# Performance work log

Hardware: AMD Instinct MI355X
Metric: run time of the kernel (lower is better)

The kernel has to match this reference:

```python
import jax, jax.numpy as jnp
import numpy as np
from jax import lax

INF = 1e12  # stands in for +inf background in the squared EDT
THRESHOLD = 0.0  # init kwarg `threshold`


def _edt1d_sq(f):
    """Exact squared Euclidean DT along last axis: d2[i] = min_j f[j] + (i-j)^2.
    Brute-force min, evaluated one output index at a time via lax.scan to keep
    memory at O(volume) instead of O(volume * n)."""
    n = f.shape[-1]
    j = jnp.arange(n, dtype=jnp.float32)

    def body(carry, i):
        d = jnp.min(f + (i - j) ** 2, axis=-1)  # [...]
        return carry, d

    _, out = lax.scan(body, None, j)  # [n, ...]
    return jnp.moveaxis(out, 0, -1)


def _edt3d(binary):
    """Euclidean distance to nearest zero voxel. binary: [B, D, H, W]."""
    f = jnp.where(binary > 0.5, INF, 0.0)
    d2 = _edt1d_sq(f)                                   # along W
    d2 = jnp.swapaxes(_edt1d_sq(jnp.swapaxes(d2, -1, -2)), -1, -2)  # along H
    d2 = jnp.moveaxis(_edt1d_sq(jnp.moveaxis(d2, 1, -1)), -1, 1)    # along D
    return jnp.sqrt(d2)


def _morse_skeleton(d, threshold):
    """Ridge / local-maximum proxy for the Morse-complex skeleton of the
    distance field: keep voxels that are 26-neighborhood maxima of d with
    d strictly above `threshold`. d: [B, D, H, W]."""
    mx = lax.reduce_window(d, -jnp.inf, lax.max,
                           (1, 3, 3, 3), (1, 1, 1, 1), 'SAME')
    return jnp.where((d >= mx) & (d > threshold), 1.0, 0.0)


def reference(img):
    # fixed discretization (reparameterize='fixed')
    img_bin = (img > 0.5).astype(jnp.float32)
    # foreground=True -> invert before distance transform
    img_bin = 1.0 - img_bin
    vol = img_bin[:, 0]                    # [B, D, H, W]
    d = _edt3d(vol)                        # distance transform, float32
    skel = _morse_skeleton(d, THRESHOLD)   # [B, D, H, W] in {0,1}
    skel = skel[:, None]                   # [B, 1, D, H, W]
    return skel * img


def setup_inputs() -> dict:
    key = jax.random.key(0)
    img = jax.random.uniform(key, (4, 1, 160, 160, 160), dtype=jnp.float32)
    return {"img": img}
```

## Files before the change

### kernel.cpp

```cpp
#include <hip/hip_runtime.h>


#define INF_F 1.0e12f

constexpr int NX = 160, NY = 160, NZ = 160, NB = 4;
constexpr int VOL   = NX * NY * NZ;
constexpr int TOTAL = NB * VOL;
constexpr int NROWS = NB * NZ * NY;
constexpr int BLK   = 256;

__device__ inline float4 f4max(float4 a, float4 b) {
    return make_float4(fmaxf(a.x, b.x), fmaxf(a.y, b.y),
                       fmaxf(a.z, b.z), fmaxf(a.w, b.w));
}

__device__ inline float edt1d_combine(int x, int lz, int rz) {
    float dl2 = (lz >= 0)   ? (float)((x - lz) * (x - lz)) : INF_F;
    float dr2 = (rz < 1000) ? (float)((rz - x) * (rz - x)) : INF_F;
    return fminf(dl2, dr2);
}

__global__ void edt_pass_x_ballot(const float* __restrict__ img,
                                  float* __restrict__ out) {
    int gw = blockIdx.x * (BLK / 64) + (threadIdx.x >> 6);
    if (gw >= NROWS) return;
    int lane = threadIdx.x & 63;
    int b = gw * NX;

    float a0 = img[b + lane];
    float a1 = img[b + 64 + lane];
    float a2 = (lane < 32) ? img[b + 128 + lane] : 0.0f;

    unsigned long long m0 = __ballot(a0 > 0.5f);
    unsigned long long m1 = __ballot(a1 > 0.5f);
    unsigned long long m2 = __ballot((lane < 32) && (a2 > 0.5f));

    const int NEG = -1048576, POS = 1048576;
    unsigned long long loMask = (~0ULL) >> (63 - lane);
    unsigned long long hiMask = (~0ULL) << lane;

    unsigned long long t;
    t = m0 & loMask;
    int lz0 = t ? (63 - __clzll(t)) : NEG;
    t = m0 & hiMask;
    int rz0 = t ? (__ffsll(t) - 1)
                : (m1 ? (64 + __ffsll(m1) - 1)
                      : (m2 ? (128 + __ffsll(m2) - 1) : POS));

    t = m1 & loMask;
    int lz1 = t ? (64 + 63 - __clzll(t))
                : (m0 ? (63 - __clzll(m0)) : NEG);
    t = m1 & hiMask;
    int rz1 = t ? (64 + __ffsll(t) - 1)
                : (m2 ? (128 + __ffsll(m2) - 1) : POS);

    t = m2 & loMask;
    int lz2 = t ? (128 + 63 - __clzll(t))
                : (m1 ? (64 + 63 - __clzll(m1))
                      : (m0 ? (63 - __clzll(m0)) : NEG));
    t = m2 & hiMask;
    int rz2 = t ? (128 + __ffsll(t) - 1) : POS;

    out[b + lane]      = edt1d_combine(lane,       lz0, rz0);
    out[b + 64 + lane] = edt1d_combine(64 + lane,  lz1, rz1);
    if (lane < 32)
        out[b + 128 + lane] = edt1d_combine(128 + lane, lz2, rz2);
}

template <int S>
__global__ void edt_pass_axis4b(const float* __restrict__ g,
                                float* __restrict__ out) {
    int tid = blockIdx.x * BLK + threadIdx.x;
    if (tid >= TOTAL / 4) return;
    int idx4 = tid * 4;
    int c = (idx4 / S) % 160;
    float4 cur = *reinterpret_cast<const float4*>(g + idx4);

    for (int base = 0; base < 159; base += 4) {
        float m = fmaxf(fmaxf(cur.x, cur.y), fmaxf(cur.z, cur.w));
        float rb2 = (float)((base + 1) * (base + 1));
        if (rb2 >= m) break;
        #pragma unroll
        for (int k = 1; k <= 4; ++k) {
            int r = base + k;
            float r2 = (float)(r * r);
            if (c - r >= 0) {
                float4 u = *reinterpret_cast<const float4*>(g + idx4 - r * S);
                cur.x = fminf(cur.x, u.x + r2); cur.y = fminf(cur.y, u.y + r2);
                cur.z = fminf(cur.z, u.z + r2); cur.w = fminf(cur.w, u.w + r2);
            }
            if (c + r < 160) {
                float4 d = *reinterpret_cast<const float4*>(g + idx4 + r * S);
                cur.x = fminf(cur.x, d.x + r2); cur.y = fminf(cur.y, d.y + r2);
                cur.z = fminf(cur.z, d.z + r2); cur.w = fminf(cur.w, d.w + r2);
            }
        }
    }
    *reinterpret_cast<float4*>(out + idx4) = cur;
}

constexpr int NX4 = NX / 4, NY2 = NY / 2, NZ2 = NZ / 2;
constexpr int NTILE = NB * NZ2 * NY2 * NX4;

__global__ void skel_kernel3(const float* __restrict__ d2,
                             const float* __restrict__ img,
                             float* __restrict__ out) {
    int tid = blockIdx.x * BLK + threadIdx.x;
    if (tid >= NTILE) return;
    int x4 = (tid % NX4) * 4;
    int t  = tid / NX4;
    int y  = (t % NY2) * 2;
    t /= NY2;
    int z  = (t % NZ2) * 2;
    int b  = t / NZ2;

    int base = ((b * NZ + z) * NY + y) * NX;
    const int yo[4] = { (y > 0) ? -NX : 0, 0, NX,
                        (y + 2 < NY) ? 2 * NX : NX };
    const int zo[4] = { (z > 0) ? -NX * NY : 0, 0, NX * NY,
                        (z + 2 < NZ) ? 2 * NX * NY : NX * NY };
    const int xl = (x4 > 0) ? x4 - 1 : 0;
    const int xr = (x4 + 4 < NX) ? x4 + 4 : NX - 1;

    float4 m[4][4];
    float  L[4][4], R[4][4];
    #pragma unroll
    for (int iz = 0; iz < 4; ++iz) {
        #pragma unroll
        for (int iy = 0; iy < 4; ++iy) {
            const float* row = d2 + base + zo[iz] + yo[iy];
            m[iz][iy] = *reinterpret_cast<const float4*>(row + x4);
            L[iz][iy] = row[xl];
            R[iz][iy] = row[xr];
        }
    }

    float4 h[4][4];
    #pragma unroll
    for (int iz = 0; iz < 4; ++iz) {
        #pragma unroll
        for (int iy = 0; iy < 4; ++iy) {
            float4 v = m[iz][iy];
            h[iz][iy] = make_float4(
                fmaxf(fmaxf(L[iz][iy], v.x), v.y),
                fmaxf(fmaxf(v.x, v.y), v.z),
                fmaxf(fmaxf(v.y, v.z), v.w),
                fmaxf(fmaxf(v.z, v.w), R[iz][iy]));
        }
    }

    float4 cm[4][2];
    #pragma unroll
    for (int iz = 0; iz < 4; ++iz) {
        cm[iz][0] = f4max(f4max(h[iz][0], h[iz][1]), h[iz][2]);
        cm[iz][1] = f4max(f4max(h[iz][1], h[iz][2]), h[iz][3]);
    }

    #pragma unroll
    for (int oz = 0; oz < 2; ++oz) {
        #pragma unroll
        for (int oy = 0; oy < 2; ++oy) {
            float4 mx = f4max(f4max(cm[oz][oy], cm[oz + 1][oy]), cm[oz + 2][oy]);
            float4 ctr = m[oz + 1][oy + 1];
            int o = base + oz * NX * NY + oy * NX + x4;
            float4 iv = *reinterpret_cast<const float4*>(img + o);
            float4 ov;
            ov.x = (ctr.x >= mx.x && ctr.x > 0.0f) ? iv.x : 0.0f;
            ov.y = (ctr.y >= mx.y && ctr.y > 0.0f) ? iv.y : 0.0f;
            ov.z = (ctr.z >= mx.z && ctr.z > 0.0f) ? iv.z : 0.0f;
            ov.w = (ctr.w >= mx.w && ctr.w > 0.0f) ? iv.w : 0.0f;
            *reinterpret_cast<float4*>(out + o) = ov;
        }
    }
}

extern "C" void kernel_launch(void* const* d_in, const int* in_sizes, int n_in,
                              void* d_out, int out_size, void* d_ws, size_t ws_size,
                              hipStream_t stream) {
    const float* img = (const float*)d_in[0];
    float* outp = (float*)d_out;
    float* ws   = (float*)d_ws;

    int gridRows = (NROWS + 3) / 4;
    int grid4    = (TOTAL / 4 + BLK - 1) / BLK;
    int gridT    = (NTILE + BLK - 1) / BLK;

    edt_pass_x_ballot<<<gridRows, BLK, 0, stream>>>(img, ws);
    edt_pass_axis4b<NX><<<grid4, BLK, 0, stream>>>(ws, outp);
    edt_pass_axis4b<NX * NY><<<grid4, BLK, 0, stream>>>(outp, ws);
    skel_kernel3<<<gridT, BLK, 0, stream>>>(ws, img, outp);
}
```

Measured before the change: 250.0 us.

## Stage full 160-length column tiles in LDS for Y and Z EDT passes

Replaces the global-memory brute-force column scan for the Y and Z passes with a block that loads a 160x16 column tile into shared memory once and scans neighbours from LDS. Each block of 640 threads covers one (batch, outer) slice and 16 x-values, and r^2 is now computed incrementally. The goal is to remove repeated uncached global/L2 reads along strided axes. In exchange it adds a block sync and large blocks, and early exit is now per thread, so wavefronts may diverge.

```diff
diff --git a/kernel.cpp b/kernel.cpp
--- a/kernel.cpp
+++ b/kernel.cpp
@@ -67,36 +67,46 @@
         out[b + 128 + lane] = edt1d_combine(128 + lane, lz2, rz2);
 }
 
-template <int S>
-__global__ void edt_pass_axis4b(const float* __restrict__ g,
-                                float* __restrict__ out) {
-    int tid = blockIdx.x * BLK + threadIdx.x;
-    if (tid >= TOTAL / 4) return;
-    int idx4 = tid * 4;
-    int c = (idx4 / S) % 160;
-    float4 cur = *reinterpret_cast<const float4*>(g + idx4);
-
-    for (int base = 0; base < 159; base += 4) {
+constexpr int XT = 16;
+constexpr int NXT = NX / XT;
+constexpr int LROW = 20;
+
+template <int S, int OSM>
+__global__ __launch_bounds__(640)
+void edt_pass_axis_lds(const float* __restrict__ g, float* __restrict__ out) {
+    __shared__ float tile[160 * LROW];
+    int t  = blockIdx.x;
+    int xt = t % NXT;
+    int o  = t / NXT;
+    int base = (o / 160) * VOL + (o % 160) * OSM + xt * XT;
+
+    int tid = threadIdx.x;
+    int xg  = tid & 3;
+    int c   = tid >> 2;
+
+    int gidx = base + c * S + xg * 4;
+    float4 cur = *reinterpret_cast<const float4*>(g + gidx);
+    *reinterpret_cast<float4*>(&tile[c * LROW + xg * 4]) = cur;
+    __syncthreads();
+
+    float r2 = 1.0f, odd = 1.0f;
+    for (int r = 1; r < 160; ++r) {
         float m = fmaxf(fmaxf(cur.x, cur.y), fmaxf(cur.z, cur.w));
-        float rb2 = (float)((base + 1) * (base + 1));
-        if (rb2 >= m) break;
-        #pragma unroll
-        for (int k = 1; k <= 4; ++k) {
-            int r = base + k;
-            float r2 = (float)(r * r);
-            if (c - r >= 0) {
-                float4 u = *reinterpret_cast<const float4*>(g + idx4 - r * S);
-                cur.x = fminf(cur.x, u.x + r2); cur.y = fminf(cur.y, u.y + r2);
-                cur.z = fminf(cur.z, u.z + r2); cur.w = fminf(cur.w, u.w + r2);
-            }
-            if (c + r < 160) {
-                float4 d = *reinterpret_cast<const float4*>(g + idx4 + r * S);
-                cur.x = fminf(cur.x, d.x + r2); cur.y = fminf(cur.y, d.y + r2);
-                cur.z = fminf(cur.z, d.z + r2); cur.w = fminf(cur.w, d.w + r2);
-            }
-        }
-    }
-    *reinterpret_cast<float4*>(out + idx4) = cur;
+        if (r2 >= m) break;
+        int cl = c - r, ch = c + r;
+        if (cl >= 0) {
+            float4 u = *reinterpret_cast<const float4*>(&tile[cl * LROW + xg * 4]);
+            cur.x = fminf(cur.x, u.x + r2); cur.y = fminf(cur.y, u.y + r2);
+            cur.z = fminf(cur.z, u.z + r2); cur.w = fminf(cur.w, u.w + r2);
+        }
+        if (ch < 160) {
+            float4 d = *reinterpret_cast<const float4*>(&tile[ch * LROW + xg * 4]);
+            cur.x = fminf(cur.x, d.x + r2); cur.y = fminf(cur.y, d.y + r2);
+            cur.z = fminf(cur.z, d.z + r2); cur.w = fminf(cur.w, d.w + r2);
+        }
+        odd += 2.0f; r2 += odd;
+    }
+    *reinterpret_cast<float4*>(out + gidx) = cur;
 }
 
 constexpr int NX4 = NX / 4, NY2 = NY / 2, NZ2 = NZ / 2;
@@ -182,11 +192,11 @@
     float* ws   = (float*)d_ws;
 
     int gridRows = (NROWS + 3) / 4;
-    int grid4    = (TOTAL / 4 + BLK - 1) / BLK;
+    int gridAx   = NB * 160 * NXT;
     int gridT    = (NTILE + BLK - 1) / BLK;
 
     edt_pass_x_ballot<<<gridRows, BLK, 0, stream>>>(img, ws);
-    edt_pass_axis4b<NX><<<grid4, BLK, 0, stream>>>(ws, outp);
-    edt_pass_axis4b<NX * NY><<<grid4, BLK, 0, stream>>>(outp, ws);
+    edt_pass_axis_lds<NX, NX * NY><<<gridAx, 640, 0, stream>>>(ws, outp);
+    edt_pass_axis_lds<NX * NY, NX><<<gridAx, 640, 0, stream>>>(outp, ws);
     skel_kernel3<<<gridT, BLK, 0, stream>>>(ws, img, outp);
 }
```

New measurement: 218.4 us. -12.6%, faster.
